# Optimization experiments

Measured on AMD Instinct MI355X. Metric: run time of the kernel, lower is better.

The kernel has to match this reference:

```python
import jax, jax.numpy as jnp
import numpy as np

B, S, HID, NH = 8, 1024, 1024, 16
HD = HID // NH  # 64
STR = 128
NEG = -1e10


def setup_inputs() -> dict:
    key = jax.random.key(0)
    ks = jax.random.split(key, 16)
    def lin(k, fan_in, fan_out):
        bound = 1.0 / np.sqrt(fan_in)
        kw, kb = jax.random.split(k)
        W = jax.random.uniform(kw, (fan_in, fan_out), jnp.float32, -bound, bound)
        b = jax.random.uniform(kb, (fan_out,), jnp.float32, -bound, bound)
        return W, b
    Wq, bq = lin(ks[0], HID, HID)
    Wk, bk = lin(ks[1], HID, HID)
    Wv, bv = lin(ks[2], HID, HID)
    Wsk, bsk = lin(ks[3], HID, STR)
    Wsv, bsv = lin(ks[4], HID, STR)
    Wo, bo = lin(ks[5], HID + STR, HID)
    return {
        "query": jax.random.normal(ks[6], (B, S, HID), jnp.float32),
        "key": jax.random.normal(ks[7], (B, S, HID), jnp.float32),
        "value": jax.random.normal(ks[8], (B, S, HID), jnp.float32),
        "x_rsa": jax.random.normal(ks[9], (B, S, STR), jnp.float32),
        "mask": jax.random.randint(ks[10], (B, 1, 1, S), 0, 2, jnp.int32),
        "rsa_mask": jax.random.randint(ks[11], (B, 1, 1, S), 0, 2, jnp.int32),
        "Wq": Wq, "bq": bq, "Wk": Wk, "bk": bk, "Wv": Wv, "bv": bv,
        "Wsk": Wsk, "bsk": bsk, "Wsv": Wsv, "bsv": bsv, "Wo": Wo, "bo": bo,
    }


def reference(query, key, value, x_rsa, mask, rsa_mask,
              Wq, bq, Wk, bk, Wv, bv, Wsk, bsk, Wsv, bsv, Wo, bo):
    scale = jnp.sqrt(jnp.float32(HD))
    Q = (query @ Wq + bq).reshape(B, S, NH, HD).transpose(0, 2, 1, 3)   # [B,NH,S,HD]
    K = (key @ Wk + bk).reshape(B, S, NH, HD).transpose(0, 2, 1, 3)
    V = (value @ Wv + bv).reshape(B, S, NH, HD).transpose(0, 2, 1, 3)
    str_K = (key @ Wsk + bsk)[:, None, :, :]    # [B,1,S,128]
    str_V = (value @ Wsv + bsv)[:, None, :, :]
    rsa_Q = x_rsa[:, None, :, :]                # [B,1,S,128]

    energy = jnp.einsum('bhqd,bhkd->bhqk', Q, K)           # [B,NH,S,S]
    rsa_energy = jnp.einsum('bhqd,bhkd->bhqk', rsa_Q, str_K)  # [B,1,S,S]
    # torch order: mask first, then divide by scale
    energy = jnp.where(mask == 0, NEG, energy) / scale
    rsa_energy = jnp.where(mask == 0, NEG, rsa_energy)
    rsa_energy = jnp.where(rsa_mask == 0, NEG, rsa_energy)  # str_scale == 1

    attention = jax.nn.softmax(energy, axis=-1)
    rsa_attention = jax.nn.softmax(rsa_energy, axis=-1)
    # dropout is identity in eval mode
    x = jnp.einsum('bhqk,bhkd->bhqd', attention, V)          # [B,NH,S,HD]
    rsa_x = jnp.einsum('bhqk,bhkd->bhqd', rsa_attention, str_V)  # [B,1,S,128]
    x = x.transpose(0, 2, 1, 3).reshape(B, S, HID)
    rsa_x = rsa_x.transpose(0, 2, 1, 3).reshape(B, S, STR)
    out = jnp.concatenate((x, rsa_x), axis=-1) @ Wo + bo     # [B,S,HID]
    return out, attention, rsa_attention
```

## Files before the change

kernel.cpp:

```cpp
#include <hip/hip_runtime.h>
#include <stdint.h>

typedef unsigned int u32;
typedef _Float16 f16_t;

typedef _Float16 f16x8 __attribute__((ext_vector_type(8)));
typedef float    f32x4 __attribute__((ext_vector_type(4)));

__device__ __forceinline__ f32x4 mfma16(f16x8 a, f16x8 b, f32x4 c){
  return __builtin_amdgcn_mfma_f32_16x16x32_f16(a, b, c, 0, 0, 0);
}
__device__ __forceinline__ float fexp2(float x){ return __builtin_amdgcn_exp2f(x); }

__device__ __forceinline__ void gl_lds16(const void* g, void* l){
  typedef const __attribute__((address_space(1))) void* gasp;
  typedef __attribute__((address_space(3))) void* lasp;
  gasp gp = reinterpret_cast<gasp>(reinterpret_cast<uintptr_t>(g));
  lasp lp = reinterpret_cast<lasp>(static_cast<u32>(reinterpret_cast<uintptr_t>(l)));
  __builtin_amdgcn_global_load_lds(gp, lp, 16, 0, 0);
}

template<int NBYTES, int ROWB, int NT>
__device__ __forceinline__ void stage_swz(const char* gbase, u32 gstrideB, char* lds, int tid){
  const u32 lane = (u32)(tid & 63);
  #pragma unroll
  for (int j = 0; j < NBYTES/(NT*16); ++j){
    u32 o   = (u32)(j*NT + tid) * 16u;
    u32 row = o / (u32)ROWB;
    u32 col = (o % (u32)ROWB) ^ ((row & ((u32)(ROWB>>4)-1u)) << 4);
    gl_lds16(gbase + (size_t)row * gstrideB + col, lds + (o - lane*16u));
  }
}

template<int ROWB>
__device__ __forceinline__ u32 swzb(u32 row, u32 col){
  return col ^ ((row & ((u32)(ROWB>>4)-1u)) << 4);
}

template<int ROWB>
__device__ __forceinline__ f16x8 frag_ld(const char* lds, u32 row, u32 kbyte){
  return *reinterpret_cast<const f16x8*>(lds + (size_t)row*ROWB + swzb<ROWB>(row, kbyte));
}

__device__ __forceinline__ void cvt8(const float* __restrict__ in, f16_t* __restrict__ out, u32 i){
  const f32x4* p = reinterpret_cast<const f32x4*>(in) + 2*(size_t)i;
  f32x4 a = p[0], b = p[1];
  f16x8 v;
  v[0]=(f16_t)a[0]; v[1]=(f16_t)a[1]; v[2]=(f16_t)a[2]; v[3]=(f16_t)a[3];
  v[4]=(f16_t)b[0]; v[5]=(f16_t)b[1]; v[6]=(f16_t)b[2]; v[7]=(f16_t)b[3];
  *(reinterpret_cast<f16x8*>(out) + i) = v;
}

__global__ void prep_all(const float* __restrict__ q, const float* __restrict__ k,
                         const float* __restrict__ v, const float* __restrict__ xr,
                         const int* __restrict__ mask, const int* __restrict__ rmask,
                         f16_t* __restrict__ qo, f16_t* __restrict__ ko,
                         f16_t* __restrict__ vo, f16_t* __restrict__ xo,
                         float* __restrict__ mb, float* __restrict__ rb,
                         const float* __restrict__ Wq, const float* __restrict__ Wk,
                         const float* __restrict__ Wv, const float* __restrict__ Wsk,
                         const float* __restrict__ Wsv, const float* __restrict__ Wo,
                         f16_t* __restrict__ wqT, f16_t* __restrict__ wkT, f16_t* __restrict__ wvT,
                         f16_t* __restrict__ wskT, f16_t* __restrict__ wsvT, f16_t* __restrict__ woT)
{
  __shared__ float tile[32][33];
  u32 b = blockIdx.x;
  if (b < 12288u){
    const float* in; f16_t* out; u32 base;
    if (b < 4096u){ in=q; out=qo; base=0u; }
    else if (b < 8192u){ in=k; out=ko; base=4096u; }
    else { in=v; out=vo; base=8192u; }
    cvt8(in, out, (b-base)*256u + threadIdx.x);
  } else if (b < 12800u){
    cvt8(xr, xo, (b-12288u)*256u + threadIdx.x);
  } else if (b < 12832u){
    u32 i = (b-12800u)*256u + threadIdx.x;
    int m = mask[i]; int r = rmask[i];
    mb[i] = m ? 0.0f : -1.0e9f;
    rb[i] = (m && r) ? 0.0f : -1.0e9f;
  } else {
    u32 t = b - 12832u;
    const float* W; f16_t* WT; u32 K, N, i, j;
    if (t < 3072u){
      u32 w = t >> 10, l = t & 1023u;
      W = w==0 ? Wq : w==1 ? Wk : Wv;
      WT = w==0 ? wqT : w==1 ? wkT : wvT;
      K = 1024u; N = 1024u; i = l & 31u; j = l >> 5;
    } else if (t < 3328u){
      u32 l = t - 3072u;
      W  = l < 128u ? Wsk : Wsv;
      WT = l < 128u ? wskT : wsvT;
      l &= 127u;
      K = 1024u; N = 128u; i = l & 31u; j = l >> 5;
    } else {
      u32 l = t - 3328u;
      W = Wo; WT = woT; K = 1152u; N = 1024u; i = l % 36u; j = l / 36u;
    }
    const u32 k0 = i*32u, n0 = j*32u;
    const int tt = threadIdx.x;
    const int r = tt >> 3, c4 = (tt & 7) * 4;
    f32x4 val = *reinterpret_cast<const f32x4*>(W + (size_t)(k0 + r)*N + n0 + c4);
    tile[r][c4+0]=val[0]; tile[r][c4+1]=val[1]; tile[r][c4+2]=val[2]; tile[r][c4+3]=val[3];
    __syncthreads();
    union { f16_t x[4]; uint64_t u; } pk;
    #pragma unroll
    for (int jj=0;jj<4;++jj) pk.x[jj] = (f16_t)tile[c4+jj][r];
    *reinterpret_cast<uint64_t*>(WT + (size_t)(n0 + r)*K + k0 + c4) = pk.u;
  }
}

struct GArg { const f16_t* A; const f16_t* Bt; const float* bias; void* C; u32 lda, ldb, ldc, K; int mode; };
struct GPack { GArg g[5]; int single; };

__global__ __launch_bounds__(256, 2)
void gemm_bt(GPack p)
{
  __shared__ char As[2][16384];
  __shared__ char Bs[2][16384];
  GArg g; u32 bn;
  const u32 bm = blockIdx.y * 128u;
  if (p.single >= 0){ g = p.g[p.single]; bn = blockIdx.x*128u; }
  else if (blockIdx.z == 0u){ if (blockIdx.x >= 2u) return; g = p.g[3u+blockIdx.x]; bn = 0u; }
  else { g = p.g[blockIdx.z-1u]; bn = blockIdx.x*128u; }

  const int tid = threadIdx.x, lane = tid & 63, wid = tid >> 6;
  const int wr = wid >> 1, wc = wid & 1;
  const char* Ab = (const char*)(g.A + (size_t)bm * g.lda);
  const char* Bb = (const char*)(g.Bt + (size_t)bn * g.ldb);
  const u32 ldaB = g.lda*2u, ldbB = g.ldb*2u;
  const bool swp = (g.mode != 2);

  f32x4 acc[4][4] = {};
  const int nt = (int)(g.K >> 6);

  stage_swz<16384,128,256>(Ab, ldaB, As[0], tid);
  stage_swz<16384,128,256>(Bb, ldbB, Bs[0], tid);
  __syncthreads();

  for (int t = 0; t < nt; ++t){
    if (t + 1 < nt){
      stage_swz<16384,128,256>(Ab + (size_t)(t+1)*128, ldaB, As[(t+1)&1], tid);
      stage_swz<16384,128,256>(Bb + (size_t)(t+1)*128, ldbB, Bs[(t+1)&1], tid);
    }
    const char* as = As[t&1]; const char* bs = Bs[t&1];
    f16x8 af[4][2], bf[4][2];
    #pragma unroll
    for (int mi=0; mi<4; ++mi)
      #pragma unroll
      for (int ks=0; ks<2; ++ks)
        af[mi][ks] = frag_ld<128>(as, (u32)(wr*64 + mi*16 + (lane&15)), (u32)(ks*64 + ((lane>>4)<<4)));
    #pragma unroll
    for (int ni=0; ni<4; ++ni)
      #pragma unroll
      for (int ks=0; ks<2; ++ks)
        bf[ni][ks] = frag_ld<128>(bs, (u32)(wc*64 + ni*16 + (lane&15)), (u32)(ks*64 + ((lane>>4)<<4)));
    if (swp){
      #pragma unroll
      for (int mi=0; mi<4; ++mi)
        #pragma unroll
        for (int ni=0; ni<4; ++ni)
          #pragma unroll
          for (int ks=0; ks<2; ++ks)
            acc[mi][ni] = mfma16(bf[ni][ks], af[mi][ks], acc[mi][ni]);
    } else {
      #pragma unroll
      for (int mi=0; mi<4; ++mi)
        #pragma unroll
        for (int ni=0; ni<4; ++ni)
          #pragma unroll
          for (int ks=0; ks<2; ++ks)
            acc[mi][ni] = mfma16(af[mi][ks], bf[ni][ks], acc[mi][ni]);
    }
    __syncthreads();
  }

  if (g.mode == 2){
    float bv[4];
    #pragma unroll
    for (int ni=0; ni<4; ++ni) bv[ni] = g.bias[bn + wc*64 + ni*16 + (lane&15)];
    f16_t* C = (f16_t*)g.C;
    #pragma unroll
    for (int mi=0; mi<4; ++mi){
      #pragma unroll
      for (int ni=0; ni<4; ++ni){
        u32 n  = bn + (u32)(wc*64 + ni*16 + (lane&15));
        u32 m0 = bm + (u32)(wr*64 + mi*16 + ((lane>>4)<<2));
        size_t idx0 = ((size_t)(m0>>10)*g.ldc + n)*1024 + (m0 & 1023);
        union { f16_t v[4]; uint64_t u; } pk;
        #pragma unroll
        for (int r=0;r<4;++r) pk.v[r] = (f16_t)(acc[mi][ni][r] + bv[ni]);
        *reinterpret_cast<uint64_t*>(C + idx0) = pk.u;
      }
    }
  } else {
    f32x4 bf4[4];
    #pragma unroll
    for (int ni=0; ni<4; ++ni)
      bf4[ni] = *reinterpret_cast<const f32x4*>(g.bias + bn + wc*64 + ni*16 + ((lane>>4)<<2));
    #pragma unroll
    for (int mi=0; mi<4; ++mi){
      u32 m = bm + (u32)(wr*64 + mi*16 + (lane&15));
      #pragma unroll
      for (int ni=0; ni<4; ++ni){
        u32 n0 = bn + (u32)(wc*64 + ni*16 + ((lane>>4)<<2));
        if (g.mode == 0){
          float* C = (float*)g.C;
          f32x4 v = acc[mi][ni] + bf4[ni];
          *reinterpret_cast<f32x4*>(C + (size_t)m*g.ldc + n0) = v;
        } else if (g.mode == 1){
          f16_t* C = (f16_t*)g.C;
          size_t idx = (((size_t)(m>>10)*16 + (n0>>6))*1024 + (m&1023))*64 + (n0&63);
          union { f16_t v[4]; uint64_t u; } pk;
          #pragma unroll
          for (int r=0;r<4;++r) pk.v[r] = (f16_t)(acc[mi][ni][r] + bf4[ni][r]);
          *reinterpret_cast<uint64_t*>(C + idx) = pk.u;
        } else {
          f16_t* C = (f16_t*)g.C;
          union { f16_t v[4]; uint64_t u; } pk;
          #pragma unroll
          for (int r=0;r<4;++r) pk.v[r] = (f16_t)(acc[mi][ni][r] + bf4[ni][r]);
          *reinterpret_cast<uint64_t*>(C + (size_t)m*g.ldc + n0) = pk.u;
        }
      }
    }
  }
}

template<int D, int KCH, int BSHIFT, int SCALEBIT>
__device__ __forceinline__ void pass1_body(char* smem,
    const f16_t* __restrict__ Qg, const f16_t* __restrict__ Kg,
    const float* __restrict__ mbias, float* __restrict__ statR,
    const int tid, const u32 qt, const u32 batch)
{
  constexpr int S = 1024;
  constexpr int ROWB = D*2;
  constexpr int MI = KCH/32;
  char* Qs  = smem;
  char* Ks0 = smem + 128*ROWB;
  char* Ks1 = Ks0 + KCH*ROWB;
  float* wsum = (float*)(Ks1 + KCH*ROWB);

  const int lane = tid & 63, wid = tid >> 6;
  const int wr = wid >> 2, wc = wid & 3;
  const float scale = SCALEBIT ? 0.1803368801111244f : 1.4426950408889634f;
  const f16_t* qb = Qg + ((size_t)batch*S + (size_t)qt*128)*D;
  const f16_t* kb = Kg + (size_t)batch*S*D;
  const float* mbb = mbias + (size_t)(batch >> BSHIFT)*S;

  stage_swz<128*ROWB, ROWB, 512>((const char*)qb, ROWB, Qs, tid);
  stage_swz<KCH*ROWB, ROWB, 512>((const char*)kb, ROWB, Ks0, tid);
  __syncthreads();

  float sacc[2] = {0.0f, 0.0f};
  constexpr int NCH = S / KCH;
  for (int ch = 0; ch < NCH; ++ch){
    if (ch + 1 < NCH)
      stage_swz<KCH*ROWB, ROWB, 512>((const char*)(kb + (size_t)(ch+1)*KCH*D), ROWB, ((ch+1)&1)?Ks1:Ks0, tid);
    const char* ks = (ch&1) ? Ks1 : Ks0;

    f32x4 mb[MI];
    #pragma unroll
    for (int mi=0; mi<MI; ++mi)
      mb[mi] = *reinterpret_cast<const f32x4*>(mbb + ch*KCH + wr*(KCH/2) + mi*16 + ((lane>>4)<<2));

    f32x4 acc[MI][2] = {};
    #pragma unroll
    for (int ksl=0; ksl<D/32; ++ksl){
      f16x8 af[MI], bf[2];
      #pragma unroll
      for (int mi=0; mi<MI; ++mi)
        af[mi] = frag_ld<ROWB>(ks, (u32)(wr*(KCH/2) + mi*16 + (lane&15)), (u32)(ksl*64 + ((lane>>4)<<4)));
      #pragma unroll
      for (int ni=0; ni<2; ++ni)
        bf[ni] = frag_ld<ROWB>(Qs, (u32)(wc*32 + ni*16 + (lane&15)), (u32)(ksl*64 + ((lane>>4)<<4)));
      #pragma unroll
      for (int mi=0; mi<MI; ++mi)
        #pragma unroll
        for (int ni=0; ni<2; ++ni)
          acc[mi][ni] = mfma16(af[mi], bf[ni], acc[mi][ni]);
    }

    #pragma unroll
    for (int ni=0; ni<2; ++ni)
      #pragma unroll
      for (int mi=0; mi<MI; ++mi)
        #pragma unroll
        for (int r=0;r<4;++r)
          sacc[ni] += fexp2(acc[mi][ni][r]*scale + mb[mi][r]);

    __syncthreads();
  }

  #pragma unroll
  for (int ni=0; ni<2; ++ni){
    float s = sacc[ni];
    s += __shfl_xor(s, 16);
    s += __shfl_xor(s, 32);
    sacc[ni] = s;
  }
  if (lane < 16){
    wsum[wr*128 + wc*32 + lane]      = sacc[0];
    wsum[wr*128 + wc*32 + 16 + lane] = sacc[1];
  }
  __syncthreads();
  if (tid < 128)
    statR[(size_t)batch*S + (size_t)qt*128 + tid] = 1.0f / (wsum[tid] + wsum[128 + tid]);
}

template<int D, int KCH, int BSHIFT, int SCALEBIT>
__device__ __forceinline__ void pass2_body(char* smem,
    const f16_t* __restrict__ Qg, const f16_t* __restrict__ Kg, const f16_t* __restrict__ Vtg,
    const float* __restrict__ mbias, const float* __restrict__ statR,
    float* __restrict__ attnOut, f16_t* __restrict__ xout, u32 xld, u32 xcolAdd,
    const int tid, const u32 qt, const u32 batch)
{
  constexpr int S = 1024;
  constexpr int ROWB = D*2;
  constexpr int ROWBV = KCH*2;
  constexpr int PROW = KCH*4;
  constexpr int MI = KCH/32;
  constexpr int MIPV = D/32;
  char* Qs  = smem;
  char* Ks0 = Qs + 128*ROWB;
  char* Ks1 = Ks0 + KCH*ROWB;
  char* Vs0 = Ks1 + KCH*ROWB;
  char* Vs1 = Vs0 + D*KCH*2;
  char* poutb = Vs1 + D*KCH*2;

  const int lane = tid & 63, wid = tid >> 6;
  const int wr = wid >> 2, wc = wid & 3;
  const u32 bb = batch >> BSHIFT;
  const float scale = SCALEBIT ? 0.1803368801111244f : 1.4426950408889634f;
  const f16_t* qb = Qg + ((size_t)batch*S + (size_t)qt*128)*D;
  const f16_t* kb = Kg + (size_t)batch*S*D;
  const char* vtb = (const char*)(Vtg + (size_t)batch*D*S);
  const float* mbb = mbias + (size_t)bb*S;

  float rreg[2];
  #pragma unroll
  for (int ni=0; ni<2; ++ni){
    u32 q = qt*128u + (u32)(wc*32 + ni*16 + (lane&15));
    rreg[ni] = statR[(size_t)batch*S + q];
  }
  f32x4 accX[MIPV][2] = {};

  stage_swz<128*ROWB, ROWB, 512>((const char*)qb, ROWB, Qs, tid);
  stage_swz<KCH*ROWB, ROWB, 512>((const char*)kb, ROWB, Ks0, tid);
  stage_swz<D*KCH*2, ROWBV, 512>(vtb, (u32)(S*2), Vs0, tid);
  __syncthreads();

  constexpr int NCH = S / KCH;
  for (int ch = 0; ch < NCH; ++ch){
    if (ch + 1 < NCH){
      stage_swz<KCH*ROWB, ROWB, 512>((const char*)(kb + (size_t)(ch+1)*KCH*D), ROWB, ((ch+1)&1)?Ks1:Ks0, tid);
      stage_swz<D*KCH*2, ROWBV, 512>(vtb + (size_t)(ch+1)*KCH*2, (u32)(S*2), ((ch+1)&1)?Vs1:Vs0, tid);
    }
    const char* ks = (ch&1) ? Ks1 : Ks0;
    const char* vs = (ch&1) ? Vs1 : Vs0;

    f32x4 mb[MI];
    #pragma unroll
    for (int mi=0; mi<MI; ++mi)
      mb[mi] = *reinterpret_cast<const f32x4*>(mbb + ch*KCH + wr*(KCH/2) + mi*16 + ((lane>>4)<<2));

    f32x4 acc[MI][2] = {};
    #pragma unroll
    for (int ksl=0; ksl<D/32; ++ksl){
      f16x8 af[MI], bf[2];
      #pragma unroll
      for (int mi=0; mi<MI; ++mi)
        af[mi] = frag_ld<ROWB>(ks, (u32)(wr*(KCH/2) + mi*16 + (lane&15)), (u32)(ksl*64 + ((lane>>4)<<4)));
      #pragma unroll
      for (int ni=0; ni<2; ++ni)
        bf[ni] = frag_ld<ROWB>(Qs, (u32)(wc*32 + ni*16 + (lane&15)), (u32)(ksl*64 + ((lane>>4)<<4)));
      #pragma unroll
      for (int mi=0; mi<MI; ++mi)
        #pragma unroll
        for (int ni=0; ni<2; ++ni)
          acc[mi][ni] = mfma16(af[mi], bf[ni], acc[mi][ni]);
    }

    #pragma unroll
    for (int ni=0; ni<2; ++ni){
      u32 q = (u32)(wc*32 + ni*16 + (lane&15));
      #pragma unroll
      for (int mi=0; mi<MI; ++mi){
        f32x4 pv;
        #pragma unroll
        for (int r=0;r<4;++r)
          pv[r] = fexp2(acc[mi][ni][r]*scale + mb[mi][r]) * rreg[ni];
        u32 k0b = (u32)(wr*(KCH/2) + mi*16 + ((lane>>4)<<2)) * 4u;
        *reinterpret_cast<f32x4*>(poutb + (size_t)q*PROW + swzb<PROW>(q, k0b)) = pv;
      }
    }
    __syncthreads();

    #pragma unroll
    for (int ksl=0; ksl<KCH/32; ++ksl){
      f16x8 pb[2];
      #pragma unroll
      for (int ni=0; ni<2; ++ni){
        u32 q = (u32)(wc*32 + ni*16 + (lane&15));
        u32 kb0 = (u32)(ksl*128 + ((lane>>4)<<5));
        f32x4 p0 = *reinterpret_cast<const f32x4*>(poutb + (size_t)q*PROW + swzb<PROW>(q, kb0));
        f32x4 p1 = *reinterpret_cast<const f32x4*>(poutb + (size_t)q*PROW + swzb<PROW>(q, kb0 + 16u));
        f16x8 v;
        v[0]=(f16_t)p0[0]; v[1]=(f16_t)p0[1]; v[2]=(f16_t)p0[2]; v[3]=(f16_t)p0[3];
        v[4]=(f16_t)p1[0]; v[5]=(f16_t)p1[1]; v[6]=(f16_t)p1[2]; v[7]=(f16_t)p1[3];
        pb[ni] = v;
      }
      #pragma unroll
      for (int mi=0; mi<MIPV; ++mi){
        f16x8 vf = frag_ld<ROWBV>(vs, (u32)(wr*(D/2) + mi*16 + (lane&15)), (u32)(ksl*64 + ((lane>>4)<<4)));
        #pragma unroll
        for (int ni=0; ni<2; ++ni)
          accX[mi][ni] = mfma16(vf, pb[ni], accX[mi][ni]);
      }
    }

    {
      u32 q2 = (u32)tid >> 2;
      float* abase = attnOut + (size_t)batch*S*S + ((size_t)qt*128 + q2)*S + (size_t)ch*KCH;
      #pragma unroll
      for (int j=0; j<KCH/16; ++j){
        u32 kbyte = ((u32)(tid&3) + 4u*(u32)j)*16u;
        f32x4 v = *reinterpret_cast<const f32x4*>(poutb + (size_t)q2*PROW + swzb<PROW>(q2, kbyte));
        *reinterpret_cast<f32x4*>(abase + (kbyte>>2)) = v;
      }
    }
    __syncthreads();
  }

  u32 col0 = (batch & ((1u<<BSHIFT)-1u)) * (u32)D + xcolAdd;
  #pragma unroll
  for (int mi=0; mi<MIPV; ++mi){
    #pragma unroll
    for (int ni=0; ni<2; ++ni){
      u32 d = (u32)(wr*(D/2) + mi*16 + ((lane>>4)<<2));
      u32 q = qt*128u + (u32)(wc*32 + ni*16 + (lane&15));
      union { f16_t v[4]; uint64_t u; } pk;
      #pragma unroll
      for (int r=0;r<4;++r) pk.v[r] = (f16_t)accX[mi][ni][r];
      *reinterpret_cast<uint64_t*>(xout + ((size_t)bb*S + q)*xld + col0 + d) = pk.u;
    }
  }
}

__global__ __launch_bounds__(512)
void attn_pass1_all(const f16_t* __restrict__ Qh, const f16_t* __restrict__ Kh,
                    const float* __restrict__ mbias, float* __restrict__ stRm,
                    const f16_t* __restrict__ xrf, const f16_t* __restrict__ strK,
                    const float* __restrict__ rbias, float* __restrict__ stRr)
{
  __shared__ char smem[50176];
  const int tid = threadIdx.x;
  const u32 qt = blockIdx.x, y = blockIdx.y;
  if (y < 8u) pass1_body<128,32,0,0>(smem, xrf, strK, rbias, stRr, tid, qt, y);
  else        pass1_body<64, 64,4,1>(smem, Qh,  Kh,   mbias, stRm, tid, qt, y-8u);
}

__global__ __launch_bounds__(512)
void attn_pass2_all(const f16_t* __restrict__ Qh, const f16_t* __restrict__ Kh,
                    const f16_t* __restrict__ Vth, const float* __restrict__ mbias,
                    const float* __restrict__ stRm, float* __restrict__ attnp,
                    const f16_t* __restrict__ xrf, const f16_t* __restrict__ strK,
                    const f16_t* __restrict__ strVt, const float* __restrict__ rbias,
                    const float* __restrict__ stRr, float* __restrict__ rsap,
                    f16_t* __restrict__ conc)
{
  __shared__ char smem[81920];
  const int tid = threadIdx.x;
  const u32 qt = blockIdx.x, y = blockIdx.y;
  if (y < 8u) pass2_body<128,32,0,0>(smem, xrf, strK, strVt, rbias, stRr, rsap, conc, 1152u, 1024u, tid, qt, y);
  else        pass2_body<64, 64,4,1>(smem, Qh,  Kh,   Vth,   mbias, stRm, attnp, conc, 1152u, 0u,    tid, qt, y-8u);
}

extern "C" void kernel_launch(void* const* d_in, const int* in_sizes, int n_in,
                              void* d_out, int out_size, void* d_ws, size_t ws_size,
                              hipStream_t stream)
{
  const float* query = (const float*)d_in[0];
  const float* key   = (const float*)d_in[1];
  const float* value = (const float*)d_in[2];
  const float* x_rsa = (const float*)d_in[3];
  const int*   mask  = (const int*)d_in[4];
  const int*   rmask = (const int*)d_in[5];
  const float* Wq = (const float*)d_in[6];  const float* bq = (const float*)d_in[7];
  const float* Wk = (const float*)d_in[8];  const float* bk = (const float*)d_in[9];
  const float* Wv = (const float*)d_in[10]; const float* bv = (const float*)d_in[11];
  const float* Wsk= (const float*)d_in[12]; const float* bsk= (const float*)d_in[13];
  const float* Wsv= (const float*)d_in[14]; const float* bsv= (const float*)d_in[15];
  const float* Wo = (const float*)d_in[16]; const float* bo = (const float*)d_in[17];

  char* ws = (char*)d_ws;
  size_t off = 0;
  auto alloc = [&](size_t bytes)->char*{ char* p = ws + off; off += (bytes + 255) & ~(size_t)255; return p; };

  f16_t* q16  = (f16_t*)alloc(16777216);
  f16_t* k16  = (f16_t*)alloc(16777216);
  f16_t* v16  = (f16_t*)alloc(16777216);
  f16_t* xrf  = (f16_t*)alloc(2097152);
  f16_t* wqT  = (f16_t*)alloc(2097152);
  f16_t* wkT  = (f16_t*)alloc(2097152);
  f16_t* wvT  = (f16_t*)alloc(2097152);
  f16_t* wskT = (f16_t*)alloc(262144);
  f16_t* wsvT = (f16_t*)alloc(262144);
  f16_t* woT  = (f16_t*)alloc(2359296);
  f16_t* Qh   = (f16_t*)alloc(16777216);
  f16_t* Kh   = (f16_t*)alloc(16777216);
  f16_t* Vth  = (f16_t*)alloc(16777216);
  f16_t* strK = (f16_t*)alloc(2097152);
  f16_t* strVt= (f16_t*)alloc(2097152);
  f16_t* conc = (f16_t*)alloc(18874368);
  float* stRm = (float*)alloc(524288);
  float* stRr = (float*)alloc(32768);
  float* mbias= (float*)alloc(32768);
  float* rbias= (float*)alloc(32768);

  prep_all<<<17312,256,0,stream>>>(query, key, value, x_rsa, mask, rmask,
                                   q16, k16, v16, xrf, mbias, rbias,
                                   Wq, Wk, Wv, Wsk, Wsv, Wo,
                                   wqT, wkT, wvT, wskT, wsvT, woT);

  {
    GPack pm{};
    pm.g[0] = {q16, wqT,  bq,  (void*)Qh,    1024u,1024u,0u,   1024u, 1};
    pm.g[1] = {k16, wkT,  bk,  (void*)Kh,    1024u,1024u,0u,   1024u, 1};
    pm.g[2] = {v16, wvT,  bv,  (void*)Vth,   1024u,1024u,1024u,1024u, 2};
    pm.g[3] = {k16, wskT, bsk, (void*)strK,  1024u,1024u,128u, 1024u, 3};
    pm.g[4] = {v16, wsvT, bsv, (void*)strVt, 1024u,1024u,128u, 1024u, 2};
    pm.single = -1;
    gemm_bt<<<dim3(8,64,4),256,0,stream>>>(pm);
  }

  float* outp  = (float*)d_out;
  float* attnp = outp + 8388608;
  float* rsap  = outp + 8388608 + 134217728;

  attn_pass1_all<<<dim3(8,136),512,0,stream>>>(Qh, Kh, mbias, stRm, xrf, strK, rbias, stRr);

  attn_pass2_all<<<dim3(8,136),512,0,stream>>>(Qh, Kh, Vth, mbias, stRm, attnp,
                                               xrf, strK, strVt, rbias, stRr, rsap, conc);

  {
    GPack po{};
    po.g[0] = {conc, woT, bo, (void*)outp, 1152u,1152u,1024u,1152u, 0};
    po.g[1] = po.g[0]; po.g[2] = po.g[0]; po.g[3] = po.g[0]; po.g[4] = po.g[0];
    po.single = 0;
    gemm_bt<<<dim3(8,64,1),256,0,stream>>>(po);
  }

  (void)in_sizes; (void)n_in; (void)out_size; (void)ws_size;
}
```

Baseline: 397.7 us.

## Keep softmax probabilities in registers via bpermute instead of LDS staging

Both attention passes now give each wave a full 16-query strip across the whole key chunk, instead of a 2x4 wave grid that split keys across waves. That removes the cross-wave LDS reduction in pass1. In pass2 the probability tile is no longer staged through LDS: the attention matrix is written straight from registers with nontemporal stores, and the PV operand is rebuilt with ds_bpermute and packed fp16 conversion. Removing the LDS buffer and a barrier per chunk cuts shared memory and lets launch bounds request higher occupancy, at the cost of less coalesced attention-matrix stores and extra permute instructions.

```diff
diff --git a/kernel.cpp b/kernel.cpp
--- a/kernel.cpp
+++ b/kernel.cpp
@@ -5,12 +5,16 @@
 typedef _Float16 f16_t;
 
 typedef _Float16 f16x8 __attribute__((ext_vector_type(8)));
+typedef __fp16   fp16x2 __attribute__((ext_vector_type(2)));
 typedef float    f32x4 __attribute__((ext_vector_type(4)));
 
 __device__ __forceinline__ f32x4 mfma16(f16x8 a, f16x8 b, f32x4 c){
   return __builtin_amdgcn_mfma_f32_16x16x32_f16(a, b, c, 0, 0, 0);
 }
 __device__ __forceinline__ float fexp2(float x){ return __builtin_amdgcn_exp2f(x); }
+__device__ __forceinline__ u32 pkrtz(float a, float b){
+  union { fp16x2 h; u32 u; } cv; cv.h = __builtin_amdgcn_cvt_pkrtz(a, b); return cv.u;
+}
 
 __device__ __forceinline__ void gl_lds16(const void* g, void* l){
   typedef const __attribute__((address_space(1))) void* gasp;
@@ -234,14 +238,14 @@
 {
   constexpr int S = 1024;
   constexpr int ROWB = D*2;
-  constexpr int MI = KCH/32;
+  constexpr int MI = KCH/16;
+  constexpr int KSL = D/32;
   char* Qs  = smem;
   char* Ks0 = smem + 128*ROWB;
   char* Ks1 = Ks0 + KCH*ROWB;
-  float* wsum = (float*)(Ks1 + KCH*ROWB);
-
-  const int lane = tid & 63, wid = tid >> 6;
-  const int wr = wid >> 2, wc = wid & 3;
+
+  const int lane = tid & 63, wq = tid >> 6;
+  const int ql = lane & 15, h = lane >> 4;
   const float scale = SCALEBIT ? 0.1803368801111244f : 1.4426950408889634f;
   const f16_t* qb = Qg + ((size_t)batch*S + (size_t)qt*128)*D;
   const f16_t* kb = Kg + (size_t)batch*S*D;
@@ -251,60 +255,36 @@
   stage_swz<KCH*ROWB, ROWB, 512>((const char*)kb, ROWB, Ks0, tid);
   __syncthreads();
 
-  float sacc[2] = {0.0f, 0.0f};
+  float sacc = 0.0f;
   constexpr int NCH = S / KCH;
   for (int ch = 0; ch < NCH; ++ch){
     if (ch + 1 < NCH)
       stage_swz<KCH*ROWB, ROWB, 512>((const char*)(kb + (size_t)(ch+1)*KCH*D), ROWB, ((ch+1)&1)?Ks1:Ks0, tid);
     const char* ks = (ch&1) ? Ks1 : Ks0;
 
-    f32x4 mb[MI];
-    #pragma unroll
-    for (int mi=0; mi<MI; ++mi)
-      mb[mi] = *reinterpret_cast<const f32x4*>(mbb + ch*KCH + wr*(KCH/2) + mi*16 + ((lane>>4)<<2));
-
-    f32x4 acc[MI][2] = {};
-    #pragma unroll
-    for (int ksl=0; ksl<D/32; ++ksl){
-      f16x8 af[MI], bf[2];
-      #pragma unroll
-      for (int mi=0; mi<MI; ++mi)
-        af[mi] = frag_ld<ROWB>(ks, (u32)(wr*(KCH/2) + mi*16 + (lane&15)), (u32)(ksl*64 + ((lane>>4)<<4)));
-      #pragma unroll
-      for (int ni=0; ni<2; ++ni)
-        bf[ni] = frag_ld<ROWB>(Qs, (u32)(wc*32 + ni*16 + (lane&15)), (u32)(ksl*64 + ((lane>>4)<<4)));
-      #pragma unroll
-      for (int mi=0; mi<MI; ++mi)
-        #pragma unroll
-        for (int ni=0; ni<2; ++ni)
-          acc[mi][ni] = mfma16(af[mi], bf[ni], acc[mi][ni]);
-    }
-
-    #pragma unroll
-    for (int ni=0; ni<2; ++ni)
-      #pragma unroll
-      for (int mi=0; mi<MI; ++mi)
-        #pragma unroll
-        for (int r=0;r<4;++r)
-          sacc[ni] += fexp2(acc[mi][ni][r]*scale + mb[mi][r]);
-
+    f32x4 acc[MI] = {};
+    #pragma unroll
+    for (int ksl=0; ksl<KSL; ++ksl){
+      f16x8 bf = frag_ld<ROWB>(Qs, (u32)(wq*16 + ql), (u32)(ksl*64 + h*16));
+      #pragma unroll
+      for (int mi=0; mi<MI; ++mi){
+        f16x8 af = frag_ld<ROWB>(ks, (u32)(mi*16 + ql), (u32)(ksl*64 + h*16));
+        acc[mi] = mfma16(af, bf, acc[mi]);
+      }
+    }
+    #pragma unroll
+    for (int mi=0; mi<MI; ++mi){
+      f32x4 mb = *reinterpret_cast<const f32x4*>(mbb + ch*KCH + mi*16 + h*4);
+      #pragma unroll
+      for (int r=0;r<4;++r) sacc += fexp2(acc[mi][r]*scale + mb[r]);
+    }
     __syncthreads();
   }
 
-  #pragma unroll
-  for (int ni=0; ni<2; ++ni){
-    float s = sacc[ni];
-    s += __shfl_xor(s, 16);
-    s += __shfl_xor(s, 32);
-    sacc[ni] = s;
-  }
-  if (lane < 16){
-    wsum[wr*128 + wc*32 + lane]      = sacc[0];
-    wsum[wr*128 + wc*32 + 16 + lane] = sacc[1];
-  }
-  __syncthreads();
-  if (tid < 128)
-    statR[(size_t)batch*S + (size_t)qt*128 + tid] = 1.0f / (wsum[tid] + wsum[128 + tid]);
+  sacc += __shfl_xor(sacc, 16);
+  sacc += __shfl_xor(sacc, 32);
+  if (lane < 16)
+    statR[(size_t)batch*S + (size_t)qt*128 + (size_t)(wq*16) + (u32)ql] = 1.0f / sacc;
 }
 
 template<int D, int KCH, int BSHIFT, int SCALEBIT>
@@ -315,20 +295,20 @@
     const int tid, const u32 qt, const u32 batch)
 {
   constexpr int S = 1024;
-  constexpr int ROWB = D*2;
+  constexpr int ROWB  = D*2;
   constexpr int ROWBV = KCH*2;
-  constexpr int PROW = KCH*4;
-  constexpr int MI = KCH/32;
-  constexpr int MIPV = D/32;
+  constexpr int MI   = KCH/16;
+  constexpr int KSL  = D/32;
+  constexpr int PSL  = KCH/32;
+  constexpr int MIPV = D/16;
   char* Qs  = smem;
   char* Ks0 = Qs + 128*ROWB;
   char* Ks1 = Ks0 + KCH*ROWB;
   char* Vs0 = Ks1 + KCH*ROWB;
-  char* Vs1 = Vs0 + D*KCH*2;
-  char* poutb = Vs1 + D*KCH*2;
-
-  const int lane = tid & 63, wid = tid >> 6;
-  const int wr = wid >> 2, wc = wid & 3;
+  char* Vs1 = Vs0 + D*ROWBV;
+
+  const int lane = tid & 63, wq = tid >> 6;
+  const int ql = lane & 15, h = lane >> 4;
   const u32 bb = batch >> BSHIFT;
   const float scale = SCALEBIT ? 0.1803368801111244f : 1.4426950408889634f;
   const f16_t* qb = Qg + ((size_t)batch*S + (size_t)qt*128)*D;
@@ -336,96 +316,65 @@
   const char* vtb = (const char*)(Vtg + (size_t)batch*D*S);
   const float* mbb = mbias + (size_t)bb*S;
 
-  float rreg[2];
-  #pragma unroll
-  for (int ni=0; ni<2; ++ni){
-    u32 q = qt*128u + (u32)(wc*32 + ni*16 + (lane&15));
-    rreg[ni] = statR[(size_t)batch*S + q];
-  }
-  f32x4 accX[MIPV][2] = {};
+  const u32 q = qt*128u + (u32)(wq*16 + ql);
+  const float rreg = statR[(size_t)batch*S + q];
+  float* arow = attnOut + (size_t)batch*S*S + (size_t)q*S;
+  f32x4 accX[MIPV] = {};
 
   stage_swz<128*ROWB, ROWB, 512>((const char*)qb, ROWB, Qs, tid);
   stage_swz<KCH*ROWB, ROWB, 512>((const char*)kb, ROWB, Ks0, tid);
-  stage_swz<D*KCH*2, ROWBV, 512>(vtb, (u32)(S*2), Vs0, tid);
+  stage_swz<D*ROWBV, ROWBV, 512>(vtb, (u32)(S*2), Vs0, tid);
   __syncthreads();
+
+  const int bidx = ((ql | ((h & 1) << 5)) << 2);
 
   constexpr int NCH = S / KCH;
   for (int ch = 0; ch < NCH; ++ch){
     if (ch + 1 < NCH){
       stage_swz<KCH*ROWB, ROWB, 512>((const char*)(kb + (size_t)(ch+1)*KCH*D), ROWB, ((ch+1)&1)?Ks1:Ks0, tid);
-      stage_swz<D*KCH*2, ROWBV, 512>(vtb + (size_t)(ch+1)*KCH*2, (u32)(S*2), ((ch+1)&1)?Vs1:Vs0, tid);
+      stage_swz<D*ROWBV, ROWBV, 512>(vtb + (size_t)(ch+1)*KCH*2, (u32)(S*2), ((ch+1)&1)?Vs1:Vs0, tid);
     }
     const char* ks = (ch&1) ? Ks1 : Ks0;
     const char* vs = (ch&1) ? Vs1 : Vs0;
 
-    f32x4 mb[MI];
-    #pragma unroll
-    for (int mi=0; mi<MI; ++mi)
-      mb[mi] = *reinterpret_cast<const f32x4*>(mbb + ch*KCH + wr*(KCH/2) + mi*16 + ((lane>>4)<<2));
-
-    f32x4 acc[MI][2] = {};
-    #pragma unroll
-    for (int ksl=0; ksl<D/32; ++ksl){
-      f16x8 af[MI], bf[2];
-      #pragma unroll
-      for (int mi=0; mi<MI; ++mi)
-        af[mi] = frag_ld<ROWB>(ks, (u32)(wr*(KCH/2) + mi*16 + (lane&15)), (u32)(ksl*64 + ((lane>>4)<<4)));
-      #pragma unroll
-      for (int ni=0; ni<2; ++ni)
-        bf[ni] = frag_ld<ROWB>(Qs, (u32)(wc*32 + ni*16 + (lane&15)), (u32)(ksl*64 + ((lane>>4)<<4)));
-      #pragma unroll
-      for (int mi=0; mi<MI; ++mi)
-        #pragma unroll
-        for (int ni=0; ni<2; ++ni)
-          acc[mi][ni] = mfma16(af[mi], bf[ni], acc[mi][ni]);
-    }
-
-    #pragma unroll
-    for (int ni=0; ni<2; ++ni){
-      u32 q = (u32)(wc*32 + ni*16 + (lane&15));
+    f32x4 acc[MI] = {};
+    #pragma unroll
+    for (int ksl=0; ksl<KSL; ++ksl){
+      f16x8 bf = frag_ld<ROWB>(Qs, (u32)(wq*16 + ql), (u32)(ksl*64 + h*16));
       #pragma unroll
       for (int mi=0; mi<MI; ++mi){
-        f32x4 pv;
-        #pragma unroll
-        for (int r=0;r<4;++r)
-          pv[r] = fexp2(acc[mi][ni][r]*scale + mb[mi][r]) * rreg[ni];
-        u32 k0b = (u32)(wr*(KCH/2) + mi*16 + ((lane>>4)<<2)) * 4u;
-        *reinterpret_cast<f32x4*>(poutb + (size_t)q*PROW + swzb<PROW>(q, k0b)) = pv;
-      }
-    }
-    __syncthreads();
-
-    #pragma unroll
-    for (int ksl=0; ksl<KCH/32; ++ksl){
-      f16x8 pb[2];
-      #pragma unroll
-      for (int ni=0; ni<2; ++ni){
-        u32 q = (u32)(wc*32 + ni*16 + (lane&15));
-        u32 kb0 = (u32)(ksl*128 + ((lane>>4)<<5));
-        f32x4 p0 = *reinterpret_cast<const f32x4*>(poutb + (size_t)q*PROW + swzb<PROW>(q, kb0));
-        f32x4 p1 = *reinterpret_cast<const f32x4*>(poutb + (size_t)q*PROW + swzb<PROW>(q, kb0 + 16u));
-        f16x8 v;
-        v[0]=(f16_t)p0[0]; v[1]=(f16_t)p0[1]; v[2]=(f16_t)p0[2]; v[3]=(f16_t)p0[3];
-        v[4]=(f16_t)p1[0]; v[5]=(f16_t)p1[1]; v[6]=(f16_t)p1[2]; v[7]=(f16_t)p1[3];
-        pb[ni] = v;
-      }
-      #pragma unroll
-      for (int mi=0; mi<MIPV; ++mi){
-        f16x8 vf = frag_ld<ROWBV>(vs, (u32)(wr*(D/2) + mi*16 + (lane&15)), (u32)(ksl*64 + ((lane>>4)<<4)));
-        #pragma unroll
-        for (int ni=0; ni<2; ++ni)
-          accX[mi][ni] = mfma16(vf, pb[ni], accX[mi][ni]);
-      }
-    }
-
-    {
-      u32 q2 = (u32)tid >> 2;
-      float* abase = attnOut + (size_t)batch*S*S + ((size_t)qt*128 + q2)*S + (size_t)ch*KCH;
-      #pragma unroll
-      for (int j=0; j<KCH/16; ++j){
-        u32 kbyte = ((u32)(tid&3) + 4u*(u32)j)*16u;
-        f32x4 v = *reinterpret_cast<const f32x4*>(poutb + (size_t)q2*PROW + swzb<PROW>(q2, kbyte));
-        *reinterpret_cast<f32x4*>(abase + (kbyte>>2)) = v;
+        f16x8 af = frag_ld<ROWB>(ks, (u32)(mi*16 + ql), (u32)(ksl*64 + h*16));
+        acc[mi] = mfma16(af, bf, acc[mi]);
+      }
+    }
+
+    u32 pk[MI][2];
+    #pragma unroll
+    for (int mi=0; mi<MI; ++mi){
+      f32x4 mb = *reinterpret_cast<const f32x4*>(mbb + ch*KCH + mi*16 + h*4);
+      f32x4 pv;
+      #pragma unroll
+      for (int r=0;r<4;++r)
+        pv[r] = fexp2(acc[mi][r]*scale + mb[r]) * rreg;
+      __builtin_nontemporal_store(pv, reinterpret_cast<f32x4*>(arow + ch*KCH + mi*16 + h*4));
+      pk[mi][0] = pkrtz(pv[0], pv[1]);
+      pk[mi][1] = pkrtz(pv[2], pv[3]);
+    }
+
+    #pragma unroll
+    for (int psl=0; psl<PSL; ++psl){
+      union { u32 w[4]; f16x8 v; } pb;
+      #pragma unroll
+      for (int s=0; s<4; ++s){
+        int ii = bidx + ((s & 2) ? 64 : 0);
+        u32 pa  = (u32)__builtin_amdgcn_ds_bpermute(ii, (int)pk[2*psl][s&1]);
+        u32 pbv = (u32)__builtin_amdgcn_ds_bpermute(ii, (int)pk[2*psl+1][s&1]);
+        pb.w[s] = (lane & 32) ? pbv : pa;
+      }
+      #pragma unroll
+      for (int mi2=0; mi2<MIPV; ++mi2){
+        f16x8 vf = frag_ld<ROWBV>(vs, (u32)(mi2*16 + ql), (u32)(psl*64 + h*16));
+        accX[mi2] = mfma16(vf, pb.v, accX[mi2]);
       }
     }
     __syncthreads();
@@ -433,33 +382,28 @@
 
   u32 col0 = (batch & ((1u<<BSHIFT)-1u)) * (u32)D + xcolAdd;
   #pragma unroll
-  for (int mi=0; mi<MIPV; ++mi){
-    #pragma unroll
-    for (int ni=0; ni<2; ++ni){
-      u32 d = (u32)(wr*(D/2) + mi*16 + ((lane>>4)<<2));
-      u32 q = qt*128u + (u32)(wc*32 + ni*16 + (lane&15));
-      union { f16_t v[4]; uint64_t u; } pk;
-      #pragma unroll
-      for (int r=0;r<4;++r) pk.v[r] = (f16_t)accX[mi][ni][r];
-      *reinterpret_cast<uint64_t*>(xout + ((size_t)bb*S + q)*xld + col0 + d) = pk.u;
-    }
-  }
-}
-
-__global__ __launch_bounds__(512)
+  for (int mi2=0; mi2<MIPV; ++mi2){
+    union { f16_t v[4]; uint64_t u; } pk4;
+    #pragma unroll
+    for (int r=0;r<4;++r) pk4.v[r] = (f16_t)accX[mi2][r];
+    *reinterpret_cast<uint64_t*>(xout + ((size_t)bb*S + q)*xld + col0 + mi2*16 + h*4) = pk4.u;
+  }
+}
+
+__global__ __launch_bounds__(512, 4)
 void attn_pass1_all(const f16_t* __restrict__ Qh, const f16_t* __restrict__ Kh,
                     const float* __restrict__ mbias, float* __restrict__ stRm,
                     const f16_t* __restrict__ xrf, const f16_t* __restrict__ strK,
                     const float* __restrict__ rbias, float* __restrict__ stRr)
 {
-  __shared__ char smem[50176];
+  __shared__ char smem[49152];
   const int tid = threadIdx.x;
   const u32 qt = blockIdx.x, y = blockIdx.y;
   if (y < 8u) pass1_body<128,32,0,0>(smem, xrf, strK, rbias, stRr, tid, qt, y);
   else        pass1_body<64, 64,4,1>(smem, Qh,  Kh,   mbias, stRm, tid, qt, y-8u);
 }
 
-__global__ __launch_bounds__(512)
+__global__ __launch_bounds__(512, 4)
 void attn_pass2_all(const f16_t* __restrict__ Qh, const f16_t* __restrict__ Kh,
                     const f16_t* __restrict__ Vth, const float* __restrict__ mbias,
                     const float* __restrict__ stRm, float* __restrict__ attnp,
@@ -468,7 +412,7 @@
                     const float* __restrict__ stRr, float* __restrict__ rsap,
                     f16_t* __restrict__ conc)
 {
-  __shared__ char smem[81920];
+  __shared__ char smem[65536];
   const int tid = threadIdx.x;
   const u32 qt = blockIdx.x, y = blockIdx.y;
   if (y < 8u) pass2_body<128,32,0,0>(smem, xrf, strK, strVt, rbias, stRr, rsap, conc, 1152u, 1024u, tid, qt, y);
```

Result: slower. 415.5 us (+4.5%).
